# Optimization experiments

Measured on AMD Instinct MI355X. Metric: run time of the kernel, lower is better.

## Reference

```python
import jax, jax.numpy as jnp
import numpy as np

DIM = 1024
HEADS = 16
HEAD_DIM = DIM // HEADS
SCALE = HEAD_DIM ** -0.5


def setup_inputs() -> dict:
    key = jax.random.key(0)
    k1, k2, k3 = jax.random.split(key, 3)
    x = jax.random.normal(k1, (4, 2048, DIM), dtype=jnp.float32)
    Wqkv = jax.random.normal(k2, (DIM, 3 * DIM), dtype=jnp.float32) * (DIM ** -0.5)
    Wout = jax.random.normal(k3, (DIM, DIM), dtype=jnp.float32) * (DIM ** -0.5)
    bout = jnp.zeros((DIM,), dtype=jnp.float32)
    return {"x": x, "Wqkv": Wqkv, "Wout": Wout, "bout": bout}


def reference(x, Wqkv, Wout, bout):
    b, n, _ = x.shape
    qkv = x @ Wqkv  # [b, n, 3*dim]
    q, k, v = jnp.split(qkv, 3, axis=-1)
    # [b, n, dim] -> [b, h, n, d]
    def split_heads(t):
        return t.reshape(b, n, HEADS, HEAD_DIM).transpose(0, 2, 1, 3)
    q, k, v = split_heads(q), split_heads(k), split_heads(v)
    dots = jnp.einsum('bhid,bhjd->bhij', q, k) * SCALE
    attn = jax.nn.softmax(dots, axis=-1)
    out = jnp.einsum('bhij,bhjd->bhid', attn, v)
    out = out.transpose(0, 2, 1, 3).reshape(b, n, DIM)
    return out @ Wout + bout  # dropout is identity in eval mode
```

## Files before the change

### kernel.cpp

```cpp
#include <hip/hip_runtime.h>
#include <hip/hip_bf16.h>

#define BATCH 4
#define SEQ   2048
#define DIM   1024
#define HEADS 16
#define HD    64
#define ROWS  (BATCH * SEQ)
#define QKV_N (3 * DIM)
#define ATT_C 0.18033688011f

typedef unsigned short u16;
typedef _Float16 half8 __attribute__((ext_vector_type(8)));
typedef _Float16 half4v __attribute__((ext_vector_type(4)));
typedef float f32x4 __attribute__((ext_vector_type(4)));
typedef unsigned int uint2v __attribute__((ext_vector_type(2)));

__device__ __forceinline__ void gload_lds16(const u16* g, u16* l) {
  typedef const __attribute__((address_space(1))) unsigned int* gp_t;
  typedef __attribute__((address_space(3))) unsigned int* lp_t;
  __builtin_amdgcn_global_load_lds((gp_t)(const void*)g, (lp_t)(void*)l, 16, 0, 0);
}

__global__ __launch_bounds__(256) void conv_x(const float* __restrict__ x,
                                              u16* __restrict__ xh) {
  int i = blockIdx.x * 256 + threadIdx.x;
  float4 v = ((const float4*)x)[i];
  half4v h = {(_Float16)v.x, (_Float16)v.y, (_Float16)v.z, (_Float16)v.w};
  *(half4v*)&xh[(size_t)i * 4] = h;
}

__global__ __launch_bounds__(256) void conv_w(const float* __restrict__ W,
                                              u16* __restrict__ Wt,
                                              int K, int N) {
  __shared__ float T[64][65];
  const int tid = threadIdx.x;
  const int k0 = blockIdx.y * 64, n0 = blockIdx.x * 64;
#pragma unroll
  for (int j = 0; j < 4; ++j) {
    int k = j * 16 + (tid >> 4), n4 = (tid & 15) * 4;
    float4 v = *(const float4*)(W + (size_t)(k0 + k) * N + n0 + n4);
    T[k][n4 + 0] = v.x; T[k][n4 + 1] = v.y; T[k][n4 + 2] = v.z; T[k][n4 + 3] = v.w;
  }
  __syncthreads();
#pragma unroll
  for (int j = 0; j < 4; ++j) {
    int n = j * 16 + (tid >> 4), k4 = (tid & 15) * 4;
    half4v w = {(_Float16)T[k4 + 0][n], (_Float16)T[k4 + 1][n],
                (_Float16)T[k4 + 2][n], (_Float16)T[k4 + 3][n]};
    *(half4v*)&Wt[(size_t)(n0 + n) * K + k0 + k4] = w;
  }
}

template <int MODE>
__global__ __launch_bounds__(256) void gemm_bt(
    const u16* __restrict__ A, const u16* __restrict__ Bt,
    const float* __restrict__ bias, void* __restrict__ Cv,
    u16* __restrict__ Qg, u16* __restrict__ Kg, u16* __restrict__ VtG,
    int M, int N, int K) {
  __shared__ u16 As[128 * 32];
  __shared__ u16 Bs[128 * 32];

  const int tid = threadIdx.x;
  const int wave = tid >> 6, lane = tid & 63;
  const int q4 = lane >> 4, c = lane & 15;
  const int wm = wave >> 1, wn = wave & 1;
  const int row0 = blockIdx.y * 128, col0 = blockIdx.x * 128;
  const int rr = lane >> 2, seg = lane & 3;

  f32x4 acc[4][4];
#pragma unroll
  for (int mi = 0; mi < 4; ++mi)
#pragma unroll
    for (int ni = 0; ni < 4; ++ni) acc[mi][ni] = (f32x4){0.f, 0.f, 0.f, 0.f};

  for (int k0 = 0; k0 < K; k0 += 32) {
#pragma unroll
    for (int i = 0; i < 2; ++i) {
      int chunk = wave * 2 + i;
      gload_lds16(A + (size_t)(row0 + chunk * 16 + rr) * K + k0 + seg * 8,
                  &As[chunk * 512]);
      gload_lds16(Bt + (size_t)(col0 + chunk * 16 + rr) * K + k0 + seg * 8,
                  &Bs[chunk * 512]);
    }
    __syncthreads();

    half8 af[4], bf[4];
#pragma unroll
    for (int mi = 0; mi < 4; ++mi)
      af[mi] = *(const half8*)&As[(wm * 64 + mi * 16 + c) * 32 + q4 * 8];
#pragma unroll
    for (int ni = 0; ni < 4; ++ni)
      bf[ni] = *(const half8*)&Bs[(wn * 64 + ni * 16 + c) * 32 + q4 * 8];
#pragma unroll
    for (int mi = 0; mi < 4; ++mi)
#pragma unroll
      for (int ni = 0; ni < 4; ++ni)
        acc[mi][ni] = __builtin_amdgcn_mfma_f32_16x16x32_f16(
            af[mi], bf[ni], acc[mi][ni], 0, 0, 0);
    __syncthreads();
  }

#pragma unroll
  for (int mi = 0; mi < 4; ++mi)
#pragma unroll
    for (int ni = 0; ni < 4; ++ni) {
      int colg = col0 + wn * 64 + ni * 16 + c;
      if (MODE == 0) {
        float bv = bias[colg];
#pragma unroll
        for (int r = 0; r < 4; ++r) {
          int rowg = row0 + wm * 64 + mi * 16 + q4 * 4 + r;
          ((float*)Cv)[(size_t)rowg * N + colg] = acc[mi][ni][r] + bv;
        }
      } else {
        int rowg0 = row0 + wm * 64 + mi * 16 + q4 * 4;
        int b  = rowg0 >> 11;
        int which = colg >> 10;
        int rem = colg & 1023;
        int hh = rem >> 6, d = rem & 63;
        size_t bh = (size_t)(b * HEADS + hh);
        if (which == 2) {
          int i0 = rowg0 & 2047;
          half4v pv = {(_Float16)acc[mi][ni][0], (_Float16)acc[mi][ni][1],
                       (_Float16)acc[mi][ni][2], (_Float16)acc[mi][ni][3]};
          *(half4v*)&VtG[(bh * HD + d) * SEQ + i0] = pv;
        } else {
          u16* dst = (which == 0) ? Qg : Kg;
          float sc = (which == 0) ? ATT_C : 1.0f;
#pragma unroll
          for (int r = 0; r < 4; ++r) {
            int i = (rowg0 + r) & 2047;
            ((_Float16*)dst)[(bh * SEQ + i) * HD + d] =
                (_Float16)(acc[mi][ni][r] * sc);
          }
        }
      }
    }
}

__global__ __launch_bounds__(512, 4) void attn_mfma(
    const u16* __restrict__ Qg, const u16* __restrict__ Kg,
    const u16* __restrict__ VtG, u16* __restrict__ ctx) {
  const int L  = blockIdx.x;
  const int bh = L & 63;
  const int b  = bh >> 4, h = bh & 15;
  const int qt = L >> 6;

  __shared__ u16 Ks[2][2][128 * 32];
  __shared__ u16 Vt[2][4][64 * 32];

  const int tid  = threadIdx.x;
  const int wave = tid >> 6;
  const int lane = tid & 63;
  const int q4   = lane >> 4;
  const int c    = lane & 15;
  const int rr   = lane >> 2, seg = lane & 3;
  const int sseg = seg ^ ((rr >> 1) & 3);
  const int xsw  = (q4 ^ ((c >> 1) & 3)) * 8;

  const size_t bhb = (size_t)bh;
  const int qrow0 = qt * 128 + wave * 16;

  half8 qf0 = *(const half8*)&Qg[(bhb * SEQ + qrow0 + c) * HD + q4 * 8];
  half8 qf1 = *(const half8*)&Qg[(bhb * SEQ + qrow0 + c) * HD + 32 + q4 * 8];

  half8 onef;
#pragma unroll
  for (int i = 0; i < 8; ++i) onef[i] = (_Float16)1.0f;

  f32x4 o_acc[4];
#pragma unroll
  for (int dt = 0; dt < 4; ++dt) o_acc[dt] = (f32x4){0.f, 0.f, 0.f, 0.f};
  f32x4 l_acc = (f32x4){0.f, 0.f, 0.f, 0.f};

  auto stage = [&](int jt, u16 (&KsB)[2][128 * 32], u16 (&VtB)[4][64 * 32]) {
    const int j0 = jt * 128;
#pragma unroll
    for (int i = 0; i < 2; ++i) {
      int chunk = wave * 2 + i;
      int kh = chunk >> 3, jr = chunk & 7;
      gload_lds16(Kg + (bhb * SEQ + j0 + jr * 16 + rr) * HD + kh * 32 + sseg * 8,
                  &KsB[kh][jr * 16 * 32]);
      int q = chunk >> 2, d16 = chunk & 3;
      gload_lds16(VtG + (bhb * HD + d16 * 16 + rr) * SEQ + j0 + q * 32 + sseg * 8,
                  &VtB[q][d16 * 16 * 32]);
    }
  };

  auto compute = [&](const u16 (&KsB)[2][128 * 32],
                     const u16 (&VtB)[4][64 * 32]) {
#pragma unroll
    for (int kc = 0; kc < 4; ++kc) {
      const int ro0 = (kc * 32 + c) * 32 + xsw;
      const int ro1 = (kc * 32 + 16 + c) * 32 + xsw;
      half8 a00 = *(const half8*)&KsB[0][ro0];
      half8 a01 = *(const half8*)&KsB[1][ro0];
      half8 a10 = *(const half8*)&KsB[0][ro1];
      half8 a11 = *(const half8*)&KsB[1][ro1];
      f32x4 st0 = (f32x4){0.f, 0.f, 0.f, 0.f};
      f32x4 st1 = (f32x4){0.f, 0.f, 0.f, 0.f};
      __builtin_amdgcn_s_setprio(1);
      st0 = __builtin_amdgcn_mfma_f32_16x16x32_f16(a00, qf0, st0, 0, 0, 0);
      st0 = __builtin_amdgcn_mfma_f32_16x16x32_f16(a01, qf1, st0, 0, 0, 0);
      st1 = __builtin_amdgcn_mfma_f32_16x16x32_f16(a10, qf0, st1, 0, 0, 0);
      st1 = __builtin_amdgcn_mfma_f32_16x16x32_f16(a11, qf1, st1, 0, 0, 0);
      __builtin_amdgcn_s_setprio(0);

      float p0 = __builtin_amdgcn_exp2f(st0[0]);
      float p1 = __builtin_amdgcn_exp2f(st0[1]);
      float p2 = __builtin_amdgcn_exp2f(st0[2]);
      float p3 = __builtin_amdgcn_exp2f(st0[3]);
      float p4 = __builtin_amdgcn_exp2f(st1[0]);
      float p5 = __builtin_amdgcn_exp2f(st1[1]);
      float p6 = __builtin_amdgcn_exp2f(st1[2]);
      float p7 = __builtin_amdgcn_exp2f(st1[3]);

      union { half4v h; unsigned int w[2]; } ea, eb;
      ea.h = (half4v){(_Float16)p0, (_Float16)p1, (_Float16)p2, (_Float16)p3};
      eb.h = (half4v){(_Float16)p4, (_Float16)p5, (_Float16)p6, (_Float16)p7};
      uint2v s0 = __builtin_amdgcn_permlane32_swap(ea.w[0], eb.w[0], false, false);
      uint2v s1 = __builtin_amdgcn_permlane32_swap(ea.w[1], eb.w[1], false, false);
      unsigned int A0 = s0[0], B0 = s0[1];
      unsigned int A1 = s1[0], B1 = s1[1];
      unsigned int Xs0 = __shfl_xor(A0, 16);
      unsigned int Xs1 = __shfl_xor(A1, 16);
      unsigned int Ys0 = __shfl_xor(B0, 16);
      unsigned int Ys1 = __shfl_xor(B1, 16);
      union { half8 h; unsigned int w[4]; } pb;
      const bool odd = (q4 & 1);
      pb.w[0] = odd ? Ys0 : A0;
      pb.w[1] = odd ? Ys1 : A1;
      pb.w[2] = odd ? B0  : Xs0;
      pb.w[3] = odd ? B1  : Xs1;

      __builtin_amdgcn_s_setprio(1);
#pragma unroll
      for (int dt = 0; dt < 4; ++dt) {
        half8 vb = *(const half8*)&VtB[kc][(dt * 16 + c) * 32 + xsw];
        o_acc[dt] = __builtin_amdgcn_mfma_f32_16x16x32_f16(
            vb, pb.h, o_acc[dt], 0, 0, 0);
      }
      l_acc = __builtin_amdgcn_mfma_f32_16x16x32_f16(onef, pb.h, l_acc, 0, 0, 0);
      __builtin_amdgcn_s_setprio(0);
    }
  };

  stage(0, Ks[0], Vt[0]);
  __syncthreads();
#pragma unroll 1
  for (int t = 0; t < 16; t += 2) {
    stage(t + 1, Ks[1], Vt[1]);
    compute(Ks[0], Vt[0]);
    __syncthreads();
    if (t + 2 < 16) stage(t + 2, Ks[0], Vt[0]);
    compute(Ks[1], Vt[1]);
    if (t + 2 < 16) __syncthreads();
  }

  float inv = 1.0f / l_acc[0];

  size_t row = (size_t)b * SEQ + qrow0 + c;
#pragma unroll
  for (int dt = 0; dt < 4; ++dt) {
    half4v o = {(_Float16)(o_acc[dt][0] * inv), (_Float16)(o_acc[dt][1] * inv),
                (_Float16)(o_acc[dt][2] * inv), (_Float16)(o_acc[dt][3] * inv)};
    *(half4v*)&((_Float16*)ctx)[row * DIM + h * HD + dt * 16 + q4 * 4] = o;
  }
}

extern "C" void kernel_launch(void* const* d_in, const int* in_sizes, int n_in,
                              void* d_out, int out_size, void* d_ws, size_t ws_size,
                              hipStream_t stream) {
  const float* x    = (const float*)d_in[0];
  const float* Wqkv = (const float*)d_in[1];
  const float* Wout = (const float*)d_in[2];
  const float* bout = (const float*)d_in[3];
  float* out = (float*)d_out;

  u16* xh   = (u16*)d_ws;
  u16* Wqt  = xh  + (size_t)ROWS * DIM;
  u16* Wot  = Wqt + (size_t)QKV_N * DIM;
  u16* Qg   = Wot + (size_t)DIM * DIM;
  u16* Kg   = Qg  + (size_t)BATCH * HEADS * SEQ * HD;
  u16* VtG  = Kg  + (size_t)BATCH * HEADS * SEQ * HD;
  u16* ctxh = VtG + (size_t)BATCH * HEADS * HD * SEQ;

  conv_x<<<ROWS * DIM / 4 / 256, 256, 0, stream>>>(x, xh);
  conv_w<<<dim3(QKV_N / 64, DIM / 64), 256, 0, stream>>>(Wqkv, Wqt, DIM, QKV_N);
  conv_w<<<dim3(DIM / 64, DIM / 64), 256, 0, stream>>>(Wout, Wot, DIM, DIM);

  gemm_bt<1><<<dim3(QKV_N / 128, ROWS / 128), 256, 0, stream>>>(
      xh, Wqt, nullptr, nullptr, Qg, Kg, VtG, ROWS, QKV_N, DIM);

  attn_mfma<<<dim3(1024), 512, 0, stream>>>(Qg, Kg, VtG, ctxh);

  gemm_bt<0><<<dim3(DIM / 128, ROWS / 128), 256, 0, stream>>>(
      ctxh, Wot, bout, out, nullptr, nullptr, nullptr, ROWS, DIM, DIM);
}
```

Measured before the change: 298.2 us.

## Process two query groups per wave to reuse K/V tiles in attention

Each wave now handles 32 query rows (two 16-row groups) instead of 16, so every K and V fragment read from LDS feeds twice as many MFMAs, and the grid is halved to 512 blocks. This cuts K/V global-to-LDS traffic and LDS reads per unit of work. The P-fragment shuffle is also rewritten to use permlane16_swap in place of the shfl_xor and select sequence. In exchange, registers per thread rise and there are fewer blocks to spread across CUs, which may lower occupancy and leave some CUs idle.

```diff
diff --git a/kernel.cpp b/kernel.cpp
--- a/kernel.cpp
+++ b/kernel.cpp
@@ -160,19 +160,28 @@
   const int xsw  = (q4 ^ ((c >> 1) & 3)) * 8;
 
   const size_t bhb = (size_t)bh;
-  const int qrow0 = qt * 128 + wave * 16;
-
-  half8 qf0 = *(const half8*)&Qg[(bhb * SEQ + qrow0 + c) * HD + q4 * 8];
-  half8 qf1 = *(const half8*)&Qg[(bhb * SEQ + qrow0 + c) * HD + 32 + q4 * 8];
+  const int qrow0 = qt * 256 + wave * 32;
+
+  half8 qf[2][2];
+#pragma unroll
+  for (int qg = 0; qg < 2; ++qg)
+#pragma unroll
+    for (int kh = 0; kh < 2; ++kh)
+      qf[qg][kh] = *(const half8*)&Qg[(bhb * SEQ + qrow0 + qg * 16 + c) * HD
+                                      + kh * 32 + q4 * 8];
 
   half8 onef;
 #pragma unroll
   for (int i = 0; i < 8; ++i) onef[i] = (_Float16)1.0f;
 
-  f32x4 o_acc[4];
-#pragma unroll
-  for (int dt = 0; dt < 4; ++dt) o_acc[dt] = (f32x4){0.f, 0.f, 0.f, 0.f};
-  f32x4 l_acc = (f32x4){0.f, 0.f, 0.f, 0.f};
+  f32x4 o_acc[2][4];
+#pragma unroll
+  for (int qg = 0; qg < 2; ++qg)
+#pragma unroll
+    for (int dt = 0; dt < 4; ++dt) o_acc[qg][dt] = (f32x4){0.f, 0.f, 0.f, 0.f};
+  f32x4 l_acc[2];
+  l_acc[0] = (f32x4){0.f, 0.f, 0.f, 0.f};
+  l_acc[1] = (f32x4){0.f, 0.f, 0.f, 0.f};
 
   auto stage = [&](int jt, u16 (&KsB)[2][128 * 32], u16 (&VtB)[4][64 * 32]) {
     const int j0 = jt * 128;
@@ -198,50 +207,50 @@
       half8 a01 = *(const half8*)&KsB[1][ro0];
       half8 a10 = *(const half8*)&KsB[0][ro1];
       half8 a11 = *(const half8*)&KsB[1][ro1];
-      f32x4 st0 = (f32x4){0.f, 0.f, 0.f, 0.f};
-      f32x4 st1 = (f32x4){0.f, 0.f, 0.f, 0.f};
-      __builtin_amdgcn_s_setprio(1);
-      st0 = __builtin_amdgcn_mfma_f32_16x16x32_f16(a00, qf0, st0, 0, 0, 0);
-      st0 = __builtin_amdgcn_mfma_f32_16x16x32_f16(a01, qf1, st0, 0, 0, 0);
-      st1 = __builtin_amdgcn_mfma_f32_16x16x32_f16(a10, qf0, st1, 0, 0, 0);
-      st1 = __builtin_amdgcn_mfma_f32_16x16x32_f16(a11, qf1, st1, 0, 0, 0);
-      __builtin_amdgcn_s_setprio(0);
-
-      float p0 = __builtin_amdgcn_exp2f(st0[0]);
-      float p1 = __builtin_amdgcn_exp2f(st0[1]);
-      float p2 = __builtin_amdgcn_exp2f(st0[2]);
-      float p3 = __builtin_amdgcn_exp2f(st0[3]);
-      float p4 = __builtin_amdgcn_exp2f(st1[0]);
-      float p5 = __builtin_amdgcn_exp2f(st1[1]);
-      float p6 = __builtin_amdgcn_exp2f(st1[2]);
-      float p7 = __builtin_amdgcn_exp2f(st1[3]);
-
-      union { half4v h; unsigned int w[2]; } ea, eb;
-      ea.h = (half4v){(_Float16)p0, (_Float16)p1, (_Float16)p2, (_Float16)p3};
-      eb.h = (half4v){(_Float16)p4, (_Float16)p5, (_Float16)p6, (_Float16)p7};
-      uint2v s0 = __builtin_amdgcn_permlane32_swap(ea.w[0], eb.w[0], false, false);
-      uint2v s1 = __builtin_amdgcn_permlane32_swap(ea.w[1], eb.w[1], false, false);
-      unsigned int A0 = s0[0], B0 = s0[1];
-      unsigned int A1 = s1[0], B1 = s1[1];
-      unsigned int Xs0 = __shfl_xor(A0, 16);
-      unsigned int Xs1 = __shfl_xor(A1, 16);
-      unsigned int Ys0 = __shfl_xor(B0, 16);
-      unsigned int Ys1 = __shfl_xor(B1, 16);
-      union { half8 h; unsigned int w[4]; } pb;
-      const bool odd = (q4 & 1);
-      pb.w[0] = odd ? Ys0 : A0;
-      pb.w[1] = odd ? Ys1 : A1;
-      pb.w[2] = odd ? B0  : Xs0;
-      pb.w[3] = odd ? B1  : Xs1;
+
+      union { half8 h; unsigned int w[4]; } pb[2];
+#pragma unroll
+      for (int qg = 0; qg < 2; ++qg) {
+        f32x4 st0 = (f32x4){0.f, 0.f, 0.f, 0.f};
+        f32x4 st1 = (f32x4){0.f, 0.f, 0.f, 0.f};
+        __builtin_amdgcn_s_setprio(1);
+        st0 = __builtin_amdgcn_mfma_f32_16x16x32_f16(a00, qf[qg][0], st0, 0, 0, 0);
+        st0 = __builtin_amdgcn_mfma_f32_16x16x32_f16(a01, qf[qg][1], st0, 0, 0, 0);
+        st1 = __builtin_amdgcn_mfma_f32_16x16x32_f16(a10, qf[qg][0], st1, 0, 0, 0);
+        st1 = __builtin_amdgcn_mfma_f32_16x16x32_f16(a11, qf[qg][1], st1, 0, 0, 0);
+        __builtin_amdgcn_s_setprio(0);
+
+        float p0 = __builtin_amdgcn_exp2f(st0[0]);
+        float p1 = __builtin_amdgcn_exp2f(st0[1]);
+        float p2 = __builtin_amdgcn_exp2f(st0[2]);
+        float p3 = __builtin_amdgcn_exp2f(st0[3]);
+        float p4 = __builtin_amdgcn_exp2f(st1[0]);
+        float p5 = __builtin_amdgcn_exp2f(st1[1]);
+        float p6 = __builtin_amdgcn_exp2f(st1[2]);
+        float p7 = __builtin_amdgcn_exp2f(st1[3]);
+
+        union { half4v h; unsigned int w[2]; } ea, eb;
+        ea.h = (half4v){(_Float16)p0, (_Float16)p1, (_Float16)p2, (_Float16)p3};
+        eb.h = (half4v){(_Float16)p4, (_Float16)p5, (_Float16)p6, (_Float16)p7};
+        uint2v t0 = __builtin_amdgcn_permlane32_swap(ea.w[0], eb.w[0], false, false);
+        uint2v t1 = __builtin_amdgcn_permlane32_swap(ea.w[1], eb.w[1], false, false);
+        uint2v u0 = __builtin_amdgcn_permlane16_swap(t0[0], t0[1], false, false);
+        uint2v u1 = __builtin_amdgcn_permlane16_swap(t1[0], t1[1], false, false);
+        pb[qg].w[0] = u0[0]; pb[qg].w[2] = u0[1];
+        pb[qg].w[1] = u1[0]; pb[qg].w[3] = u1[1];
+      }
 
       __builtin_amdgcn_s_setprio(1);
 #pragma unroll
       for (int dt = 0; dt < 4; ++dt) {
         half8 vb = *(const half8*)&VtB[kc][(dt * 16 + c) * 32 + xsw];
-        o_acc[dt] = __builtin_amdgcn_mfma_f32_16x16x32_f16(
-            vb, pb.h, o_acc[dt], 0, 0, 0);
+        o_acc[0][dt] = __builtin_amdgcn_mfma_f32_16x16x32_f16(
+            vb, pb[0].h, o_acc[0][dt], 0, 0, 0);
+        o_acc[1][dt] = __builtin_amdgcn_mfma_f32_16x16x32_f16(
+            vb, pb[1].h, o_acc[1][dt], 0, 0, 0);
       }
-      l_acc = __builtin_amdgcn_mfma_f32_16x16x32_f16(onef, pb.h, l_acc, 0, 0, 0);
+      l_acc[0] = __builtin_amdgcn_mfma_f32_16x16x32_f16(onef, pb[0].h, l_acc[0], 0, 0, 0);
+      l_acc[1] = __builtin_amdgcn_mfma_f32_16x16x32_f16(onef, pb[1].h, l_acc[1], 0, 0, 0);
       __builtin_amdgcn_s_setprio(0);
     }
   };
@@ -258,14 +267,18 @@
     if (t + 2 < 16) __syncthreads();
   }
 
-  float inv = 1.0f / l_acc[0];
-
-  size_t row = (size_t)b * SEQ + qrow0 + c;
-#pragma unroll
-  for (int dt = 0; dt < 4; ++dt) {
-    half4v o = {(_Float16)(o_acc[dt][0] * inv), (_Float16)(o_acc[dt][1] * inv),
-                (_Float16)(o_acc[dt][2] * inv), (_Float16)(o_acc[dt][3] * inv)};
-    *(half4v*)&((_Float16*)ctx)[row * DIM + h * HD + dt * 16 + q4 * 4] = o;
+#pragma unroll
+  for (int qg = 0; qg < 2; ++qg) {
+    float inv = 1.0f / l_acc[qg][0];
+    size_t row = (size_t)b * SEQ + qrow0 + qg * 16 + c;
+#pragma unroll
+    for (int dt = 0; dt < 4; ++dt) {
+      half4v o = {(_Float16)(o_acc[qg][dt][0] * inv),
+                  (_Float16)(o_acc[qg][dt][1] * inv),
+                  (_Float16)(o_acc[qg][dt][2] * inv),
+                  (_Float16)(o_acc[qg][dt][3] * inv)};
+      *(half4v*)&((_Float16*)ctx)[row * DIM + h * HD + dt * 16 + q4 * 4] = o;
+    }
   }
 }
 
@@ -293,7 +306,7 @@
   gemm_bt<1><<<dim3(QKV_N / 128, ROWS / 128), 256, 0, stream>>>(
       xh, Wqt, nullptr, nullptr, Qg, Kg, VtG, ROWS, QKV_N, DIM);
 
-  attn_mfma<<<dim3(1024), 512, 0, stream>>>(Qg, Kg, VtG, ctxh);
+  attn_mfma<<<dim3(512), 512, 0, stream>>>(Qg, Kg, VtG, ctxh);
 
   gemm_bt<0><<<dim3(DIM / 128, ROWS / 128), 256, 0, stream>>>(
       ctxh, Wot, bout, out, nullptr, nullptr, nullptr, ROWS, DIM, DIM);
```

After: 276.9 us. 1.08x faster.
